# Kernel tuning notes

Hardware: AMD Instinct MI355X
Metric: run time of the kernel (lower is better)

The kernel has to match this reference:

```python
import jax, jax.numpy as jnp
import numpy as np

N_NODES = 50000
N_EDGES = 1600000
LORA_R = 8


def gcn_conv(h, W, b, src, dst, n):
    # PyG GCNConv: linear transform, add self-loops, symmetric normalization,
    # scatter-add aggregation at target nodes, then bias.
    h = h @ W  # [N, out]
    ones = jnp.ones(src.shape[0], dtype=h.dtype)
    deg = jax.ops.segment_sum(ones, dst, num_segments=n) + 1.0  # +1 for self-loop
    dis = jax.lax.rsqrt(deg)  # deg >= 1 always
    norm = dis[src] * dis[dst]  # [E]
    agg = jax.ops.segment_sum(norm[:, None] * h[src], dst, num_segments=n)
    agg = agg + (dis * dis)[:, None] * h  # self-loop contribution
    return agg + b


def lora(h, A, B):
    # LoRALinear: b(a(x)) * (1/r); replaces input (not additive)
    return (h @ A) @ B * (1.0 / LORA_R)


def setup_inputs() -> dict:
    key = jax.random.key(0)
    ks = jax.random.split(key, 12)
    inp = {}
    inp['x'] = jax.random.normal(ks[0], (N_NODES, 128), dtype=jnp.float32)
    inp['edge_index'] = jax.random.randint(ks[1], (2, N_EDGES), 0, N_NODES, dtype=jnp.int64 if jax.config.jax_enable_x64 else jnp.int32)
    inp['domain_idx'] = jax.random.randint(ks[2], (N_NODES,), 0, 3, dtype=jnp.int32)
    inp['emb_table'] = jax.random.normal(ks[3], (3, 4096), dtype=jnp.float32)
    s1 = 1.0 / np.sqrt(4224.0)
    inp['W1'] = jax.random.normal(ks[4], (4224, 32), dtype=jnp.float32) * s1
    inp['b1'] = jnp.zeros((32,), dtype=jnp.float32)
    inp['A1'] = jax.random.normal(ks[5], (32, LORA_R), dtype=jnp.float32) * (1.0 / np.sqrt(32.0))
    inp['B1'] = jax.random.normal(ks[6], (LORA_R, 32), dtype=jnp.float32) * (1.0 / np.sqrt(LORA_R))
    inp['W2'] = jax.random.normal(ks[7], (32, 5), dtype=jnp.float32) * (1.0 / np.sqrt(32.0))
    inp['b2'] = jnp.zeros((5,), dtype=jnp.float32)
    inp['A2'] = jax.random.normal(ks[8], (5, LORA_R), dtype=jnp.float32) * (1.0 / np.sqrt(5.0))
    inp['B2'] = jax.random.normal(ks[9], (LORA_R, 5), dtype=jnp.float32) * (1.0 / np.sqrt(LORA_R))
    return inp


def reference(x, edge_index, domain_idx, emb_table, W1, b1, A1, B1, W2, b2, A2, B2):
    n = x.shape[0]
    src, dst = edge_index[0], edge_index[1]
    embedded = emb_table[domain_idx]  # [N, 4096]
    h = jnp.concatenate([embedded, x], axis=1)  # [N, 4224]
    h = gcn_conv(h, W1, b1, src, dst, n)
    h = lora(h, A1, B1)
    h = jax.nn.relu(h)
    h = gcn_conv(h, W2, b2, src, dst, n)
    h = lora(h, A2, B2)
    return jax.nn.log_softmax(h, axis=1)
```

## Files before the change

### kernel.cpp

```cpp
#include <hip/hip_runtime.h>
#include <hip/hip_bf16.h>
#include <hip/hip_fp16.h>


#define XDIM 128
#define EMBDIM 4096
#define TB 4096
#define BSH 6
#define BN 64
#define ECAP2 2560
#define MAXT 512

__global__ void __launch_bounds__(256) kA(
    const int* __restrict__ src, const int* __restrict__ dst,
    unsigned int* __restrict__ tedges, unsigned int* __restrict__ toffcnt,
    int e, int ntiles,
    const float* __restrict__ emb, const float* __restrict__ W1,
    float* __restrict__ emb_part,
    const float* __restrict__ A1, const float* __restrict__ A2,
    const float* __restrict__ B2, const float* __restrict__ b1,
    float* __restrict__ M2, float* __restrict__ b1A1,
    const float* __restrict__ x, float* __restrict__ g, int n) {
    __shared__ __align__(16) char smem[24576];
    int t = threadIdx.x, bx = blockIdx.x;
    if (bx < ntiles) {
        unsigned int* staged = (unsigned int*)smem;
        int* loff = (int*)(smem + 16384);
        int* rctr = (int*)(smem + 20480);
        int base = bx * TB;
        int len = min(TB, e - base);
        for (int i = t; i < 1024; i += 256) { loff[i] = 0; rctr[i] = 0; }
        __syncthreads();
        int sreg[16], dreg[16];
        #pragma unroll
        for (int k = 0; k < 16; ++k) {
            int i = t + k * 256;
            if (i < len) {
                sreg[k] = src[base + i];
                dreg[k] = dst[base + i];
            }
        }
        #pragma unroll
        for (int k = 0; k < 16; ++k) {
            int i = t + k * 256;
            if (i < len) atomicAdd(&loff[dreg[k] >> BSH], 1);
        }
        __syncthreads();
        if (t < 64) {
            int ch = t * 16;
            int v[16]; int s0 = 0;
            #pragma unroll
            for (int k = 0; k < 16; ++k) { v[k] = loff[ch + k]; s0 += v[k]; }
            int pre = s0;
            #pragma unroll
            for (int d2 = 1; d2 < 64; d2 <<= 1) {
                int up = __shfl_up(pre, d2);
                if (t >= d2) pre += up;
            }
            int excl = pre - s0;
            unsigned int* ocp = toffcnt + (size_t)bx * 1024 + ch;
            #pragma unroll
            for (int k = 0; k < 16; ++k) {
                loff[ch + k] = excl;
                ocp[k] = ((unsigned int)excl << 16) | (unsigned int)v[k];
                excl += v[k];
            }
        }
        __syncthreads();
        #pragma unroll
        for (int k = 0; k < 16; ++k) {
            int i = t + k * 256;
            if (i < len) {
                int b = dreg[k] >> BSH;
                int r = atomicAdd(&rctr[b], 1);
                staged[loff[b] + r] = ((unsigned int)dreg[k] << 16) | (unsigned int)sreg[k];
            }
        }
        __syncthreads();
        uint4* tw = (uint4*)(tedges + (size_t)bx * TB);
        const uint4* sr = (const uint4*)staged;
        int lw = (len + 3) >> 2;
        for (int i = t; i < lw; i += 256) tw[i] = sr[i];
    } else if (bx < ntiles + 96) {
        float* red = (float*)smem;
        int bx2 = bx - ntiles;
        int dm = bx2 >> 5, seg = bx2 & 31;
        const float* er = emb + dm * EMBDIM + seg * 128;
        const float* wr = W1 + (size_t)(seg * 128) * 32;
        int j = t & 31, kk = t >> 5;
        float acc = 0.f;
        for (int k2 = kk; k2 < 128; k2 += 8) acc += er[k2] * wr[k2 * 32 + j];
        red[kk * 32 + j] = acc;
        __syncthreads();
        if (t < 32) {
            float s = 0.f;
            #pragma unroll
            for (int r = 0; r < 8; ++r) s += red[r * 32 + t];
            emb_part[bx2 * 32 + t] = s;
        }
        if (bx2 == 0) {
            if (t < 25) {
                int c = t / 5, cp = t % 5;
                float s = 0.f;
                #pragma unroll
                for (int r = 0; r < 8; ++r) s += A2[c * 8 + r] * B2[r * 5 + cp];
                M2[c * 5 + cp] = s * 0.125f;
            }
            if (t >= 32 && t < 40) {
                int j2 = t - 32;
                float s = 0.f;
                #pragma unroll
                for (int k = 0; k < 32; ++k) s += b1[k] * A1[k * 8 + j2];
                b1A1[j2] = s;
            }
        }
    } else {
        __half* xsh = (__half*)smem;
        float* sWA  = (float*)(smem + 16384);
        float* sA1  = (float*)(smem + 20480);
        int gb = bx - ntiles - 96;
        int row0 = gb * 64;
        sA1[t] = A1[t];
        for (int i = t; i < 2048; i += 256) {
            int row = i >> 5, c4 = i & 31;
            int gi = row0 + row;
            float4 v = (gi < n) ? ((const float4*)x)[(size_t)gi * 32 + c4]
                                : make_float4(0.f, 0.f, 0.f, 0.f);
            __half2 h01 = __floats2half2_rn(v.x, v.y);
            __half2 h23 = __floats2half2_rn(v.z, v.w);
            uint2 pk;
            pk.x = *(unsigned int*)&h01;
            pk.y = *(unsigned int*)&h23;
            *(uint2*)(xsh + row * 128 + c4 * 4) = pk;
        }
        __syncthreads();
        for (int idx = t; idx < 1024; idx += 256) {
            int k = idx >> 3, j = idx & 7;
            const float* wr = W1 + (size_t)(EMBDIM + k) * 32;
            float s = 0.f;
            #pragma unroll 8
            for (int c = 0; c < 32; ++c) s += wr[c] * sA1[c * 8 + j];
            sWA[idx] = s;
        }
        __syncthreads();
        int row = t >> 3, j = t & 7;
        const __half2* xr1 = (const __half2*)(xsh + row * 128);
        const __half2* xr2 = (const __half2*)(xsh + (row + 32) * 128);
        float acc1 = 0.f, acc2 = 0.f;
        #pragma unroll 8
        for (int k2 = 0; k2 < 64; ++k2) {
            float2 fa = __half22float2(xr1[k2]);
            float2 fb = __half22float2(xr2[k2]);
            float w0 = sWA[(2 * k2) * 8 + j];
            float w1 = sWA[(2 * k2 + 1) * 8 + j];
            acc1 += fa.x * w0 + fa.y * w1;
            acc2 += fb.x * w0 + fb.y * w1;
        }
        int gi1 = row0 + row, gi2 = row0 + row + 32;
        if (gi1 < n) g[(size_t)gi1 * 8 + j] = acc1;
        if (gi2 < n) g[(size_t)gi2 * 8 + j] = acc2;
    }
}

__global__ void __launch_bounds__(256) kB(
    const unsigned int* __restrict__ tedges, const unsigned int* __restrict__ toffcnt,
    int ntiles,
    const float* __restrict__ emb_part, const float* __restrict__ A1,
    const int* __restrict__ dom, const float* __restrict__ g,
    int* __restrict__ deg, __half* __restrict__ p1h,
    unsigned short* __restrict__ nsrc, unsigned int* __restrict__ bm, int n) {
    __shared__ int hist[64], eoff[64], rctr[64], sdom[64];
    __shared__ int mtot;
    __shared__ unsigned short rbase[MAXT], soff[MAXT], slen[MAXT];
    __shared__ float sA1[256], sproj[96], sembA1[24];
    __shared__ __align__(16) unsigned int ebuf[ECAP2];
    __shared__ __align__(16) unsigned short esrc[ECAP2];
    int t = threadIdx.x, b = blockIdx.x;
    int row0 = b << BSH;
    if (t < 64) {
        hist[t] = 0; rctr[t] = 0;
        int gi = row0 + t;
        sdom[t] = (gi < n) ? dom[gi] : 0;
    }
    sA1[t] = A1[t];
    if (t < 96) {
        int dm = t >> 5, c = t & 31;
        float s = 0.f;
        #pragma unroll
        for (int seg = 0; seg < 32; ++seg) s += emb_part[(dm * 32 + seg) * 32 + c];
        sproj[dm * 32 + c] = s;
    }
    if (t < 64) {
        int carry = 0;
        int nch = (ntiles + 63) >> 6;
        for (int c = 0; c < nch; ++c) {
            int idx = (c << 6) + t;
            unsigned int oc = (idx < ntiles) ? toffcnt[(size_t)idx * 1024 + b] : 0u;
            int l = (int)(oc & 0xffffu);
            int pre = l;
            #pragma unroll
            for (int d2 = 1; d2 < 64; d2 <<= 1) {
                int up = __shfl_up(pre, d2);
                if (t >= d2) pre += up;
            }
            if (idx < ntiles) {
                rbase[idx] = (unsigned short)min(carry + pre - l, 65535);
                soff[idx]  = (unsigned short)(oc >> 16);
                slen[idx]  = (unsigned short)l;
            }
            carry += __shfl(pre, 63);
        }
        if (t == 0) mtot = carry;
    }
    __syncthreads();
    int m = mtot;
    if (m > ECAP2) m = ECAP2;
    if (t == 0) bm[b] = (unsigned int)m;
    {
        int g4 = t >> 2, l4 = t & 3;
        for (int tl = g4; tl < ntiles; tl += 64) {
            int l = slen[tl];
            if (l > 0) {
                const unsigned int* rp = tedges + (size_t)tl * TB + soff[tl];
                int bse = rbase[tl];
                for (int j = l4; j < l; j += 4) {
                    int p = bse + j;
                    if (p < ECAP2) ebuf[p] = rp[j];
                }
            }
        }
    }
    __syncthreads();
    for (int i = t; i < m; i += 256) atomicAdd(&hist[(ebuf[i] >> 16) & (BN - 1)], 1);
    __syncthreads();
    if (t < 64) {
        int v = hist[t];
        int pre = v;
        #pragma unroll
        for (int d2 = 1; d2 < 64; d2 <<= 1) {
            int up = __shfl_up(pre, d2);
            if (t >= d2) pre += up;
        }
        eoff[t] = pre - v;
        int gi = row0 + t;
        if (gi < n) deg[gi] = v;
    } else if (t < 88) {
        int dm = (t - 64) >> 3, j = (t - 64) & 7;
        float s = 0.f;
        #pragma unroll 8
        for (int c = 0; c < 32; ++c) s += sproj[dm * 32 + c] * sA1[c * 8 + j];
        sembA1[dm * 8 + j] = s;
    }
    __syncthreads();
    for (int i = t; i < m; i += 256) {
        unsigned int u = ebuf[i];
        int dl = (int)(u >> 16) & (BN - 1);
        int r = atomicAdd(&rctr[dl], 1);
        esrc[eoff[dl] + r] = (unsigned short)(u & 0xffffu);
    }
    for (int i = t; i < 512; i += 256) {
        int row = i >> 3, j = i & 7;
        int gi = row0 + row;
        if (gi < n) {
            float dd = rsqrtf((float)(hist[row] + 1));
            float v = g[(size_t)gi * 8 + j] + sembA1[sdom[row] * 8 + j];
            p1h[(size_t)gi * 8 + j] = __float2half_rn(dd * v);
        }
    }
    __syncthreads();
    {
        uint4* npw = (uint4*)(nsrc + (size_t)b * ECAP2);
        const uint4* ew = (const uint4*)esrc;
        int mw = (m + 7) >> 3;
        for (int i = t; i < mw; i += 256) npw[i] = ew[i];
    }
}

__global__ void __launch_bounds__(256) k_bagg1(
    const __half* __restrict__ p1h, const unsigned short* __restrict__ nsrc,
    const unsigned int* __restrict__ bm, const int* __restrict__ deg,
    const float* __restrict__ b1A1, const float* __restrict__ B1,
    const float* __restrict__ W2, __half* __restrict__ qh, int n) {
    __shared__ __align__(16) unsigned short esrc[ECAP2];
    __shared__ int eoff[BN], sdeg[BN];
    __shared__ float pacc[3][BN][8];
    __shared__ float sB1[256], sW2[160], sb[8];
    int t = threadIdx.x, b = blockIdx.x;
    int node0 = b << BSH;
    sB1[t] = B1[t];
    if (t < 160) sW2[t] = W2[t];
    if (t < 8) sb[t] = b1A1[t];
    if (t < 64) {
        int node = node0 + t;
        int v = (node < n) ? deg[node] : 0;
        sdeg[t] = v;
        int pre = v;
        #pragma unroll
        for (int d2 = 1; d2 < 64; d2 <<= 1) {
            int up = __shfl_up(pre, d2);
            if (t >= d2) pre += up;
        }
        eoff[t] = pre - v;
    }
    __syncthreads();
    int m = (int)bm[b];
    if (m > ECAP2) m = ECAP2;
    {
        const uint4* npw = (const uint4*)(nsrc + (size_t)b * ECAP2);
        uint4* ew = (uint4*)esrc;
        int mw = (m + 7) >> 3;
        for (int i = t; i < mw; i += 256) ew[i] = npw[i];
    }
    __syncthreads();
    int nodeL = t & (BN - 1), tsub = t >> BSH;
    int base0 = eoff[nodeL], c = sdeg[nodeL];
    float a[8] = {0.f, 0.f, 0.f, 0.f, 0.f, 0.f, 0.f, 0.f};
    float a2[8] = {0.f, 0.f, 0.f, 0.f, 0.f, 0.f, 0.f, 0.f};
    int k = tsub;
    for (; k + 4 < c; k += 8) {
        int s1 = esrc[base0 + k], s2 = esrc[base0 + k + 4];
        uint4 u = *(const uint4*)(p1h + (size_t)s1 * 8);
        uint4 v = *(const uint4*)(p1h + (size_t)s2 * 8);
        float2 f;
        f = __half22float2(*(__half2*)&u.x); a[0] += f.x; a[1] += f.y;
        f = __half22float2(*(__half2*)&u.y); a[2] += f.x; a[3] += f.y;
        f = __half22float2(*(__half2*)&u.z); a[4] += f.x; a[5] += f.y;
        f = __half22float2(*(__half2*)&u.w); a[6] += f.x; a[7] += f.y;
        f = __half22float2(*(__half2*)&v.x); a2[0] += f.x; a2[1] += f.y;
        f = __half22float2(*(__half2*)&v.y); a2[2] += f.x; a2[3] += f.y;
        f = __half22float2(*(__half2*)&v.z); a2[4] += f.x; a2[5] += f.y;
        f = __half22float2(*(__half2*)&v.w); a2[6] += f.x; a2[7] += f.y;
    }
    for (; k < c; k += 4) {
        int s1 = esrc[base0 + k];
        uint4 u = *(const uint4*)(p1h + (size_t)s1 * 8);
        float2 f;
        f = __half22float2(*(__half2*)&u.x); a[0] += f.x; a[1] += f.y;
        f = __half22float2(*(__half2*)&u.y); a[2] += f.x; a[3] += f.y;
        f = __half22float2(*(__half2*)&u.z); a[4] += f.x; a[5] += f.y;
        f = __half22float2(*(__half2*)&u.w); a[6] += f.x; a[7] += f.y;
    }
    #pragma unroll
    for (int j = 0; j < 8; ++j) a[j] += a2[j];
    if (tsub > 0) {
        #pragma unroll
        for (int j = 0; j < 8; ++j) pacc[tsub - 1][nodeL][j] = a[j];
    }
    __syncthreads();
    if (t < BN) {
        int node = node0 + t;
        if (node < n) {
            float dd = rsqrtf((float)(sdeg[t] + 1));
            uint4 u = *(const uint4*)(p1h + (size_t)node * 8);
            float2 f;
            float af[8];
            f = __half22float2(*(__half2*)&u.x); af[0] = a[0] + f.x; af[1] = a[1] + f.y;
            f = __half22float2(*(__half2*)&u.y); af[2] = a[2] + f.x; af[3] = a[3] + f.y;
            f = __half22float2(*(__half2*)&u.z); af[4] = a[4] + f.x; af[5] = a[5] + f.y;
            f = __half22float2(*(__half2*)&u.w); af[6] = a[6] + f.x; af[7] = a[7] + f.y;
            #pragma unroll
            for (int ps = 0; ps < 3; ++ps) {
                #pragma unroll
                for (int j = 0; j < 8; ++j) af[j] += pacc[ps][t][j];
            }
            #pragma unroll
            for (int j = 0; j < 8; ++j) af[j] = dd * af[j] + sb[j];
            float qv[5] = {0.f, 0.f, 0.f, 0.f, 0.f};
            #pragma unroll
            for (int c2 = 0; c2 < 32; ++c2) {
                float tv = 0.f;
                #pragma unroll
                for (int j = 0; j < 8; ++j) tv += af[j] * sB1[j * 32 + c2];
                float st = fmaxf(tv * 0.125f, 0.f);
                #pragma unroll
                for (int o = 0; o < 5; ++o) qv[o] += st * sW2[c2 * 5 + o];
            }
            #pragma unroll
            for (int o = 0; o < 5; ++o) qh[(size_t)node * 8 + o] = __float2half_rn(dd * qv[o]);
        }
    }
}

__global__ void __launch_bounds__(256) k_bagg2(
    const __half* __restrict__ qh, const unsigned short* __restrict__ nsrc,
    const unsigned int* __restrict__ bm, const int* __restrict__ deg,
    const float* __restrict__ b2, const float* __restrict__ M2,
    float* __restrict__ out, int n) {
    __shared__ __align__(16) unsigned short esrc[ECAP2];
    __shared__ int eoff[BN], sdeg[BN];
    __shared__ float pacc[3][BN][5];
    __shared__ float sM2[25], sb2[5];
    int t = threadIdx.x, b = blockIdx.x;
    int node0 = b << BSH;
    if (t < 25) sM2[t] = M2[t];
    if (t < 5) sb2[t] = b2[t];
    if (t < 64) {
        int node = node0 + t;
        int v = (node < n) ? deg[node] : 0;
        sdeg[t] = v;
        int pre = v;
        #pragma unroll
        for (int d2 = 1; d2 < 64; d2 <<= 1) {
            int up = __shfl_up(pre, d2);
            if (t >= d2) pre += up;
        }
        eoff[t] = pre - v;
    }
    __syncthreads();
    int m = (int)bm[b];
    if (m > ECAP2) m = ECAP2;
    {
        const uint4* npw = (const uint4*)(nsrc + (size_t)b * ECAP2);
        uint4* ew = (uint4*)esrc;
        int mw = (m + 7) >> 3;
        for (int i = t; i < mw; i += 256) ew[i] = npw[i];
    }
    __syncthreads();
    int nodeL = t & (BN - 1), tsub = t >> BSH;
    int base0 = eoff[nodeL], c = sdeg[nodeL];
    float a[5] = {0.f, 0.f, 0.f, 0.f, 0.f};
    float a2[5] = {0.f, 0.f, 0.f, 0.f, 0.f};
    int k = tsub;
    for (; k + 4 < c; k += 8) {
        int s1 = esrc[base0 + k], s2 = esrc[base0 + k + 4];
        uint4 u = *(const uint4*)(qh + (size_t)s1 * 8);
        uint4 v = *(const uint4*)(qh + (size_t)s2 * 8);
        float2 f;
        f = __half22float2(*(__half2*)&u.x); a[0] += f.x; a[1] += f.y;
        f = __half22float2(*(__half2*)&u.y); a[2] += f.x; a[3] += f.y;
        f = __half22float2(*(__half2*)&u.z); a[4] += f.x;
        f = __half22float2(*(__half2*)&v.x); a2[0] += f.x; a2[1] += f.y;
        f = __half22float2(*(__half2*)&v.y); a2[2] += f.x; a2[3] += f.y;
        f = __half22float2(*(__half2*)&v.z); a2[4] += f.x;
    }
    for (; k < c; k += 4) {
        int s1 = esrc[base0 + k];
        uint4 u = *(const uint4*)(qh + (size_t)s1 * 8);
        float2 f;
        f = __half22float2(*(__half2*)&u.x); a[0] += f.x; a[1] += f.y;
        f = __half22float2(*(__half2*)&u.y); a[2] += f.x; a[3] += f.y;
        f = __half22float2(*(__half2*)&u.z); a[4] += f.x;
    }
    #pragma unroll
    for (int j = 0; j < 5; ++j) a[j] += a2[j];
    if (tsub > 0) {
        #pragma unroll
        for (int j = 0; j < 5; ++j) pacc[tsub - 1][nodeL][j] = a[j];
    }
    __syncthreads();
    if (t < BN) {
        int node = node0 + t;
        if (node < n) {
            float dd = rsqrtf((float)(sdeg[t] + 1));
            uint4 u = *(const uint4*)(qh + (size_t)node * 8);
            float2 f;
            float av[5];
            f = __half22float2(*(__half2*)&u.x); av[0] = a[0] + f.x; av[1] = a[1] + f.y;
            f = __half22float2(*(__half2*)&u.y); av[2] = a[2] + f.x; av[3] = a[3] + f.y;
            f = __half22float2(*(__half2*)&u.z); av[4] = a[4] + f.x;
            #pragma unroll
            for (int ps = 0; ps < 3; ++ps) {
                #pragma unroll
                for (int j = 0; j < 5; ++j) av[j] += pacc[ps][t][j];
            }
            #pragma unroll
            for (int j = 0; j < 5; ++j) av[j] = dd * av[j] + sb2[j];
            float z[5];
            #pragma unroll
            for (int cp = 0; cp < 5; ++cp) {
                float s = 0.f;
                #pragma unroll
                for (int c2 = 0; c2 < 5; ++c2) s += av[c2] * sM2[c2 * 5 + cp];
                z[cp] = s;
            }
            float mx = z[0];
            #pragma unroll
            for (int c2 = 1; c2 < 5; ++c2) mx = fmaxf(mx, z[c2]);
            float ssum = 0.f;
            #pragma unroll
            for (int c2 = 0; c2 < 5; ++c2) ssum += __expf(z[c2] - mx);
            float ls = __logf(ssum);
            #pragma unroll
            for (int c2 = 0; c2 < 5; ++c2) out[node * 5 + c2] = z[c2] - mx - ls;
        }
    }
}

extern "C" void kernel_launch(void* const* d_in, const int* in_sizes, int n_in,
                              void* d_out, int out_size, void* d_ws, size_t ws_size,
                              hipStream_t stream) {
    const float* x   = (const float*)d_in[0];
    const int*   ei  = (const int*)d_in[1];
    const int*   dom = (const int*)d_in[2];
    const float* emb = (const float*)d_in[3];
    const float* W1  = (const float*)d_in[4];
    const float* b1  = (const float*)d_in[5];
    const float* A1  = (const float*)d_in[6];
    const float* B1  = (const float*)d_in[7];
    const float* W2  = (const float*)d_in[8];
    const float* b2  = (const float*)d_in[9];
    const float* A2  = (const float*)d_in[10];
    const float* B2  = (const float*)d_in[11];
    float* out = (float*)d_out;

    int n = in_sizes[2];
    int e = in_sizes[1] / 2;
    const int* src = ei;
    const int* dst = ei + e;

    int ntiles = (e + TB - 1) / TB;
    int nbuck  = (n + BN - 1) >> BSH;
    int ngb    = (n + 63) / 64;

    char* base = (char*)d_ws;
    size_t o = 0;
    auto carve = [&](size_t bytes) {
        void* p = base + o;
        o = (o + bytes + 15) & ~(size_t)15;
        return p;
    };
    float* emb_part = (float*)carve(96 * 32 * sizeof(float));
    float* M2       = (float*)carve(32 * sizeof(float));
    float* b1A1     = (float*)carve(8 * sizeof(float));
    unsigned int* bm = (unsigned int*)carve(1024 * sizeof(int));
    int*   deg      = (int*)carve((size_t)n * sizeof(int));
    float* g        = (float*)carve((size_t)n * 8 * sizeof(float));
    __half* p1h     = (__half*)carve((size_t)n * 8 * sizeof(__half));
    __half* qh      = (__half*)carve((size_t)n * 8 * sizeof(__half));
    unsigned int* tedges  = (unsigned int*)carve((size_t)ntiles * TB * sizeof(unsigned int));
    unsigned int* toffcnt = (unsigned int*)carve((size_t)ntiles * 1024 * sizeof(unsigned int));
    unsigned short* nsrc  = (unsigned short*)carve((size_t)nbuck * ECAP2 * sizeof(unsigned short));
    (void)ws_size; (void)n_in; (void)out_size;

    kA<<<ntiles + 96 + ngb, 256, 0, stream>>>(
        src, dst, tedges, toffcnt, e, ntiles,
        emb, W1, emb_part, A1, A2, B2, b1, M2, b1A1, x, g, n);
    kB<<<nbuck, 256, 0, stream>>>(tedges, toffcnt, ntiles, emb_part, A1, dom, g,
                                  deg, p1h, nsrc, bm, n);
    k_bagg1<<<nbuck, 256, 0, stream>>>(p1h, nsrc, bm, deg, b1A1, B1, W2, qh, n);
    k_bagg2<<<nbuck, 256, 0, stream>>>(qh, nsrc, bm, deg, b2, M2, out, n);
}
```

Baseline: 149.3 us.

## Fuse x·(W1A1) projection into bucket kernel, parallelize tile scan, deepen gather unroll

```diff
diff --git a/kernel.cpp b/kernel.cpp
--- a/kernel.cpp
+++ b/kernel.cpp
@@ -20,7 +20,7 @@
     const float* __restrict__ A1, const float* __restrict__ A2,
     const float* __restrict__ B2, const float* __restrict__ b1,
     float* __restrict__ M2, float* __restrict__ b1A1,
-    const float* __restrict__ x, float* __restrict__ g, int n) {
+    float* __restrict__ WA, int n) {
     __shared__ __align__(16) char smem[24576];
     int t = threadIdx.x, bx = blockIdx.x;
     if (bx < ntiles) {
@@ -115,24 +115,8 @@
             }
         }
     } else {
-        __half* xsh = (__half*)smem;
-        float* sWA  = (float*)(smem + 16384);
-        float* sA1  = (float*)(smem + 20480);
-        int gb = bx - ntiles - 96;
-        int row0 = gb * 64;
+        float* sA1 = (float*)smem;
         sA1[t] = A1[t];
-        for (int i = t; i < 2048; i += 256) {
-            int row = i >> 5, c4 = i & 31;
-            int gi = row0 + row;
-            float4 v = (gi < n) ? ((const float4*)x)[(size_t)gi * 32 + c4]
-                                : make_float4(0.f, 0.f, 0.f, 0.f);
-            __half2 h01 = __floats2half2_rn(v.x, v.y);
-            __half2 h23 = __floats2half2_rn(v.z, v.w);
-            uint2 pk;
-            pk.x = *(unsigned int*)&h01;
-            pk.y = *(unsigned int*)&h23;
-            *(uint2*)(xsh + row * 128 + c4 * 4) = pk;
-        }
         __syncthreads();
         for (int idx = t; idx < 1024; idx += 256) {
             int k = idx >> 3, j = idx & 7;
@@ -140,25 +124,8 @@
             float s = 0.f;
             #pragma unroll 8
             for (int c = 0; c < 32; ++c) s += wr[c] * sA1[c * 8 + j];
-            sWA[idx] = s;
-        }
-        __syncthreads();
-        int row = t >> 3, j = t & 7;
-        const __half2* xr1 = (const __half2*)(xsh + row * 128);
-        const __half2* xr2 = (const __half2*)(xsh + (row + 32) * 128);
-        float acc1 = 0.f, acc2 = 0.f;
-        #pragma unroll 8
-        for (int k2 = 0; k2 < 64; ++k2) {
-            float2 fa = __half22float2(xr1[k2]);
-            float2 fb = __half22float2(xr2[k2]);
-            float w0 = sWA[(2 * k2) * 8 + j];
-            float w1 = sWA[(2 * k2 + 1) * 8 + j];
-            acc1 += fa.x * w0 + fa.y * w1;
-            acc2 += fb.x * w0 + fb.y * w1;
-        }
-        int gi1 = row0 + row, gi2 = row0 + row + 32;
-        if (gi1 < n) g[(size_t)gi1 * 8 + j] = acc1;
-        if (gi2 < n) g[(size_t)gi2 * 8 + j] = acc2;
+            WA[idx] = s;
+        }
     }
 }
 
@@ -166,13 +133,14 @@
     const unsigned int* __restrict__ tedges, const unsigned int* __restrict__ toffcnt,
     int ntiles,
     const float* __restrict__ emb_part, const float* __restrict__ A1,
-    const int* __restrict__ dom, const float* __restrict__ g,
+    const int* __restrict__ dom, const float* __restrict__ x,
+    const float* __restrict__ WA,
     int* __restrict__ deg, __half* __restrict__ p1h,
     unsigned short* __restrict__ nsrc, unsigned int* __restrict__ bm, int n) {
     __shared__ int hist[64], eoff[64], rctr[64], sdom[64];
-    __shared__ int mtot;
+    __shared__ int wtot[4];
     __shared__ unsigned short rbase[MAXT], soff[MAXT], slen[MAXT];
-    __shared__ float sA1[256], sproj[96], sembA1[24];
+    __shared__ float sA1[256], sWA[1024], sproj[96], sembA1[24];
     __shared__ __align__(16) unsigned int ebuf[ECAP2];
     __shared__ __align__(16) unsigned short esrc[ECAP2];
     int t = threadIdx.x, b = blockIdx.x;
@@ -183,6 +151,8 @@
         sdom[t] = (gi < n) ? dom[gi] : 0;
     }
     sA1[t] = A1[t];
+    #pragma unroll
+    for (int q = 0; q < 4; ++q) sWA[t + q * 256] = WA[t + q * 256];
     if (t < 96) {
         int dm = t >> 5, c = t & 31;
         float s = 0.f;
@@ -190,30 +160,39 @@
         for (int seg = 0; seg < 32; ++seg) s += emb_part[(dm * 32 + seg) * 32 + c];
         sproj[dm * 32 + c] = s;
     }
-    if (t < 64) {
-        int carry = 0;
-        int nch = (ntiles + 63) >> 6;
-        for (int c = 0; c < nch; ++c) {
-            int idx = (c << 6) + t;
-            unsigned int oc = (idx < ntiles) ? toffcnt[(size_t)idx * 1024 + b] : 0u;
-            int l = (int)(oc & 0xffffu);
-            int pre = l;
-            #pragma unroll
-            for (int d2 = 1; d2 < 64; d2 <<= 1) {
-                int up = __shfl_up(pre, d2);
-                if (t >= d2) pre += up;
-            }
-            if (idx < ntiles) {
-                rbase[idx] = (unsigned short)min(carry + pre - l, 65535);
-                soff[idx]  = (unsigned short)(oc >> 16);
-                slen[idx]  = (unsigned short)l;
-            }
-            carry += __shfl(pre, 63);
-        }
-        if (t == 0) mtot = carry;
-    }
-    __syncthreads();
-    int m = mtot;
+    {
+        int w = t >> 6, l = t & 63;
+        int i0 = w * 128 + l, i1 = w * 128 + 64 + l;
+        unsigned int oc0 = (i0 < ntiles) ? toffcnt[(size_t)i0 * 1024 + b] : 0u;
+        unsigned int oc1 = (i1 < ntiles) ? toffcnt[(size_t)i1 * 1024 + b] : 0u;
+        int l0 = (int)(oc0 & 0xffffu), l1 = (int)(oc1 & 0xffffu);
+        int p0 = l0, p1 = l1;
+        #pragma unroll
+        for (int d2 = 1; d2 < 64; d2 <<= 1) {
+            int u0 = __shfl_up(p0, d2);
+            int u1 = __shfl_up(p1, d2);
+            if (l >= d2) { p0 += u0; p1 += u1; }
+        }
+        int totA = __shfl(p0, 63);
+        if (l == 63) wtot[w] = p0 + p1;
+        __syncthreads();
+        int woff = 0;
+        #pragma unroll
+        for (int q = 0; q < 4; ++q) woff += (q < w) ? wtot[q] : 0;
+        if (i0 < ntiles) {
+            rbase[i0] = (unsigned short)min(woff + p0 - l0, 65535);
+            soff[i0]  = (unsigned short)(oc0 >> 16);
+            slen[i0]  = (unsigned short)l0;
+        }
+        if (i1 < ntiles) {
+            rbase[i1] = (unsigned short)min(woff + totA + p1 - l1, 65535);
+            soff[i1]  = (unsigned short)(oc1 >> 16);
+            slen[i1]  = (unsigned short)l1;
+        }
+        if (t == 0) wtot[0] = wtot[0] + wtot[1] + wtot[2] + wtot[3];
+    }
+    __syncthreads();
+    int m = wtot[0];
     if (m > ECAP2) m = ECAP2;
     if (t == 0) bm[b] = (unsigned int)m;
     {
@@ -262,9 +241,19 @@
         int row = i >> 3, j = i & 7;
         int gi = row0 + row;
         if (gi < n) {
+            const float4* xr = (const float4*)x + (size_t)gi * 32;
+            float acc = 0.f;
+            #pragma unroll 8
+            for (int c4 = 0; c4 < 32; ++c4) {
+                float4 v = xr[c4];
+                acc += v.x * sWA[(c4 * 4 + 0) * 8 + j]
+                     + v.y * sWA[(c4 * 4 + 1) * 8 + j]
+                     + v.z * sWA[(c4 * 4 + 2) * 8 + j]
+                     + v.w * sWA[(c4 * 4 + 3) * 8 + j];
+            }
             float dd = rsqrtf((float)(hist[row] + 1));
-            float v = g[(size_t)gi * 8 + j] + sembA1[sdom[row] * 8 + j];
-            p1h[(size_t)gi * 8 + j] = __float2half_rn(dd * v);
+            float val = acc + sembA1[sdom[row] * 8 + j];
+            p1h[(size_t)gi * 8 + j] = __float2half_rn(dd * val);
         }
     }
     __syncthreads();
@@ -314,9 +303,34 @@
     __syncthreads();
     int nodeL = t & (BN - 1), tsub = t >> BSH;
     int base0 = eoff[nodeL], c = sdeg[nodeL];
-    float a[8] = {0.f, 0.f, 0.f, 0.f, 0.f, 0.f, 0.f, 0.f};
-    float a2[8] = {0.f, 0.f, 0.f, 0.f, 0.f, 0.f, 0.f, 0.f};
+    float a[8] = {0,0,0,0,0,0,0,0}, a2[8] = {0,0,0,0,0,0,0,0};
+    float a3[8] = {0,0,0,0,0,0,0,0}, a4[8] = {0,0,0,0,0,0,0,0};
     int k = tsub;
+    for (; k + 12 < c; k += 16) {
+        int s1 = esrc[base0 + k],     s2 = esrc[base0 + k + 4];
+        int s3 = esrc[base0 + k + 8], s4 = esrc[base0 + k + 12];
+        uint4 u = *(const uint4*)(p1h + (size_t)s1 * 8);
+        uint4 v = *(const uint4*)(p1h + (size_t)s2 * 8);
+        uint4 w = *(const uint4*)(p1h + (size_t)s3 * 8);
+        uint4 y = *(const uint4*)(p1h + (size_t)s4 * 8);
+        float2 f;
+        f = __half22float2(*(__half2*)&u.x); a[0] += f.x; a[1] += f.y;
+        f = __half22float2(*(__half2*)&u.y); a[2] += f.x; a[3] += f.y;
+        f = __half22float2(*(__half2*)&u.z); a[4] += f.x; a[5] += f.y;
+        f = __half22float2(*(__half2*)&u.w); a[6] += f.x; a[7] += f.y;
+        f = __half22float2(*(__half2*)&v.x); a2[0] += f.x; a2[1] += f.y;
+        f = __half22float2(*(__half2*)&v.y); a2[2] += f.x; a2[3] += f.y;
+        f = __half22float2(*(__half2*)&v.z); a2[4] += f.x; a2[5] += f.y;
+        f = __half22float2(*(__half2*)&v.w); a2[6] += f.x; a2[7] += f.y;
+        f = __half22float2(*(__half2*)&w.x); a3[0] += f.x; a3[1] += f.y;
+        f = __half22float2(*(__half2*)&w.y); a3[2] += f.x; a3[3] += f.y;
+        f = __half22float2(*(__half2*)&w.z); a3[4] += f.x; a3[5] += f.y;
+        f = __half22float2(*(__half2*)&w.w); a3[6] += f.x; a3[7] += f.y;
+        f = __half22float2(*(__half2*)&y.x); a4[0] += f.x; a4[1] += f.y;
+        f = __half22float2(*(__half2*)&y.y); a4[2] += f.x; a4[3] += f.y;
+        f = __half22float2(*(__half2*)&y.z); a4[4] += f.x; a4[5] += f.y;
+        f = __half22float2(*(__half2*)&y.w); a4[6] += f.x; a4[7] += f.y;
+    }
     for (; k + 4 < c; k += 8) {
         int s1 = esrc[base0 + k], s2 = esrc[base0 + k + 4];
         uint4 u = *(const uint4*)(p1h + (size_t)s1 * 8);
@@ -341,7 +355,7 @@
         f = __half22float2(*(__half2*)&u.w); a[6] += f.x; a[7] += f.y;
     }
     #pragma unroll
-    for (int j = 0; j < 8; ++j) a[j] += a2[j];
+    for (int j = 0; j < 8; ++j) a[j] += a2[j] + a3[j] + a4[j];
     if (tsub > 0) {
         #pragma unroll
         for (int j = 0; j < 8; ++j) pacc[tsub - 1][nodeL][j] = a[j];
@@ -418,9 +432,30 @@
     __syncthreads();
     int nodeL = t & (BN - 1), tsub = t >> BSH;
     int base0 = eoff[nodeL], c = sdeg[nodeL];
-    float a[5] = {0.f, 0.f, 0.f, 0.f, 0.f};
-    float a2[5] = {0.f, 0.f, 0.f, 0.f, 0.f};
+    float a[5] = {0,0,0,0,0}, a2[5] = {0,0,0,0,0};
+    float a3[5] = {0,0,0,0,0}, a4[5] = {0,0,0,0,0};
     int k = tsub;
+    for (; k + 12 < c; k += 16) {
+        int s1 = esrc[base0 + k],     s2 = esrc[base0 + k + 4];
+        int s3 = esrc[base0 + k + 8], s4 = esrc[base0 + k + 12];
+        uint4 u = *(const uint4*)(qh + (size_t)s1 * 8);
+        uint4 v = *(const uint4*)(qh + (size_t)s2 * 8);
+        uint4 w = *(const uint4*)(qh + (size_t)s3 * 8);
+        uint4 y = *(const uint4*)(qh + (size_t)s4 * 8);
+        float2 f;
+        f = __half22float2(*(__half2*)&u.x); a[0] += f.x; a[1] += f.y;
+        f = __half22float2(*(__half2*)&u.y); a[2] += f.x; a[3] += f.y;
+        f = __half22float2(*(__half2*)&u.z); a[4] += f.x;
+        f = __half22float2(*(__half2*)&v.x); a2[0] += f.x; a2[1] += f.y;
+        f = __half22float2(*(__half2*)&v.y); a2[2] += f.x; a2[3] += f.y;
+        f = __half22float2(*(__half2*)&v.z); a2[4] += f.x;
+        f = __half22float2(*(__half2*)&w.x); a3[0] += f.x; a3[1] += f.y;
+        f = __half22float2(*(__half2*)&w.y); a3[2] += f.x; a3[3] += f.y;
+        f = __half22float2(*(__half2*)&w.z); a3[4] += f.x;
+        f = __half22float2(*(__half2*)&y.x); a4[0] += f.x; a4[1] += f.y;
+        f = __half22float2(*(__half2*)&y.y); a4[2] += f.x; a4[3] += f.y;
+        f = __half22float2(*(__half2*)&y.z); a4[4] += f.x;
+    }
     for (; k + 4 < c; k += 8) {
         int s1 = esrc[base0 + k], s2 = esrc[base0 + k + 4];
         uint4 u = *(const uint4*)(qh + (size_t)s1 * 8);
@@ -442,7 +477,7 @@
         f = __half22float2(*(__half2*)&u.z); a[4] += f.x;
     }
     #pragma unroll
-    for (int j = 0; j < 5; ++j) a[j] += a2[j];
+    for (int j = 0; j < 5; ++j) a[j] += a2[j] + a3[j] + a4[j];
     if (tsub > 0) {
         #pragma unroll
         for (int j = 0; j < 5; ++j) pacc[tsub - 1][nodeL][j] = a[j];
@@ -510,7 +545,6 @@
 
     int ntiles = (e + TB - 1) / TB;
     int nbuck  = (n + BN - 1) >> BSH;
-    int ngb    = (n + 63) / 64;
 
     char* base = (char*)d_ws;
     size_t o = 0;
@@ -522,9 +556,9 @@
     float* emb_part = (float*)carve(96 * 32 * sizeof(float));
     float* M2       = (float*)carve(32 * sizeof(float));
     float* b1A1     = (float*)carve(8 * sizeof(float));
+    float* WA       = (float*)carve(1024 * sizeof(float));
     unsigned int* bm = (unsigned int*)carve(1024 * sizeof(int));
     int*   deg      = (int*)carve((size_t)n * sizeof(int));
-    float* g        = (float*)carve((size_t)n * 8 * sizeof(float));
     __half* p1h     = (__half*)carve((size_t)n * 8 * sizeof(__half));
     __half* qh      = (__half*)carve((size_t)n * 8 * sizeof(__half));
     unsigned int* tedges  = (unsigned int*)carve((size_t)ntiles * TB * sizeof(unsigned int));
@@ -532,11 +566,11 @@
     unsigned short* nsrc  = (unsigned short*)carve((size_t)nbuck * ECAP2 * sizeof(unsigned short));
     (void)ws_size; (void)n_in; (void)out_size;
 
-    kA<<<ntiles + 96 + ngb, 256, 0, stream>>>(
+    kA<<<ntiles + 97, 256, 0, stream>>>(
         src, dst, tedges, toffcnt, e, ntiles,
-        emb, W1, emb_part, A1, A2, B2, b1, M2, b1A1, x, g, n);
-    kB<<<nbuck, 256, 0, stream>>>(tedges, toffcnt, ntiles, emb_part, A1, dom, g,
-                                  deg, p1h, nsrc, bm, n);
+        emb, W1, emb_part, A1, A2, B2, b1, M2, b1A1, WA, n);
+    kB<<<nbuck, 256, 0, stream>>>(tedges, toffcnt, ntiles, emb_part, A1, dom,
+                                  x, WA, deg, p1h, nsrc, bm, n);
     k_bagg1<<<nbuck, 256, 0, stream>>>(p1h, nsrc, bm, deg, b1A1, B1, W2, qh, n);
     k_bagg2<<<nbuck, 256, 0, stream>>>(qh, nsrc, bm, deg, b2, M2, out, n);
 }
```

Measured after the change: 148.4 us. About the same (-0.6%).
